# Performance work log

Hardware: AMD Instinct MI355X
Metric: run time of the kernel (lower is better)

The kernel has to match this reference:

```python
import jax, jax.numpy as jnp
import numpy as np

# Config mirroring sample_tokens(temperature=1.0, top_p=0.9, top_k=50, neg_entropy=True)
TEMPERATURE = 1.0
TOP_P = 0.9
TOP_K = 50
EPS = 1e-10


def _top_p_filter(logits, top_p):
    # Descending sort over vocab, cumulative softmax mass, shift-by-one keep rule.
    order = jnp.argsort(-logits, axis=-1)                      # [N, V]
    sorted_logits = jnp.take_along_axis(logits, order, axis=-1)
    cum = jnp.cumsum(jax.nn.softmax(sorted_logits, axis=-1), axis=-1)
    remove = cum > top_p
    # torch: sorted_indices_to_remove[...,1:] = [...,:-1]; [...,0] = 0
    remove = jnp.concatenate([jnp.zeros_like(remove[..., :1]), remove[..., :-1]], axis=-1)
    rows = jnp.arange(logits.shape[0])[:, None]
    mask = jnp.zeros(logits.shape, dtype=bool).at[rows, order].set(remove)
    return jnp.where(mask, jnp.finfo(logits.dtype).min, logits)


def _top_k_filter(logits, k):
    kth = jax.lax.top_k(logits, k)[0][..., -1:]                # k-th largest per row
    return jnp.where(logits < kth, jnp.finfo(logits.dtype).min, logits)


def setup_inputs() -> dict:
    key = jax.random.key(0)
    logits = jax.random.normal(key, (1024, 128000), dtype=jnp.float32) * 2.0
    return {"logits": logits}


def reference(logits):
    # temperature > 0 path
    z = logits / TEMPERATURE
    z = _top_p_filter(z, TOP_P)
    z = _top_k_filter(z, TOP_K)
    probs = jax.nn.softmax(z, axis=-1)                         # [N, V]
    # Categorical sample (softmax-invariant: categorical on filtered logits)
    x0 = jax.random.categorical(jax.random.key(42), z, axis=-1)  # [N] int
    initial_confidence = jnp.take_along_axis(probs, x0[:, None], axis=-1)[:, 0]
    # neg_entropy confidence: sum p * log(p + eps) over vocab
    confidence = jnp.sum(probs * jnp.log(probs + EPS), axis=-1)
    return confidence, x0, initial_confidence
```

## Files before the change

kernel.cpp:

```cpp
#include <hip/hip_runtime.h>
#include <stdint.h>


#define ROWS   1024
#define VOCAB  128000
#define CAP    2048
#define KTOP   50
#define TOPP   0.9f
#define NTHR   256
#define T0     6.0f

typedef float fx4 __attribute__((ext_vector_type(4)));

__device__ __forceinline__ void tf_round(uint32_t& x0, uint32_t& x1, int r) {
  x0 += x1;
  x1 = (x1 << r) | (x1 >> (32 - r));
  x1 ^= x0;
}

__device__ __forceinline__ uint32_t threefry_bits(uint32_t lin) {
  const uint32_t ks0 = 0u;
  const uint32_t ks1 = 42u;
  const uint32_t ks2 = 0x1BD11BDAu ^ 0u ^ 42u;
  uint32_t x0 = 0u + ks0, x1 = lin + ks1;
  tf_round(x0,x1,13); tf_round(x0,x1,15); tf_round(x0,x1,26); tf_round(x0,x1,6);
  x0 += ks1; x1 += ks2 + 1u;
  tf_round(x0,x1,17); tf_round(x0,x1,29); tf_round(x0,x1,16); tf_round(x0,x1,24);
  x0 += ks2; x1 += ks0 + 2u;
  tf_round(x0,x1,13); tf_round(x0,x1,15); tf_round(x0,x1,26); tf_round(x0,x1,6);
  x0 += ks0; x1 += ks1 + 3u;
  tf_round(x0,x1,17); tf_round(x0,x1,29); tf_round(x0,x1,16); tf_round(x0,x1,24);
  x0 += ks1; x1 += ks2 + 4u;
  tf_round(x0,x1,13); tf_round(x0,x1,15); tf_round(x0,x1,26); tf_round(x0,x1,6);
  x0 += ks2; x1 += ks0 + 5u;
  return x0 ^ x1;
}

__device__ __forceinline__ float gumbel_at(uint32_t lin) {
  uint32_t bits = threefry_bits(lin);
  float f = __uint_as_float((bits >> 9) | 0x3F800000u) - 1.0f;
  float u = f + 1.17549435e-38f;
  return -logf(-logf(u));
}

__global__ __launch_bounds__(NTHR, 4) void sampler_kernel(
    const float* __restrict__ logits, float* __restrict__ out) {
  const int row = blockIdx.x;
  const int tid = threadIdx.x;
  const float* __restrict__ rowp = logits + (size_t)row * VOCAB;

  __shared__ float cand_val[CAP];
  __shared__ int   cand_idx[CAP];
  __shared__ float red_a[NTHR];
  __shared__ float red_b[NTHR];
  __shared__ int   red_i[NTHR];
  __shared__ int   s_cnt;
  __shared__ float s_topv[KTOP];
  __shared__ int   s_tops[KTOP];

  if (tid == 0) s_cnt = 0;
  __syncthreads();

  float m0 = -__builtin_inff(), m1 = -__builtin_inff();
  float s0 = 0.f, s1 = 0.f, s2 = 0.f, s3 = 0.f;

  const fx4* __restrict__ rowp4 = reinterpret_cast<const fx4*>(rowp);

#define PROCESS(v, f4idx)                                                     \
  do {                                                                        \
    s0 += __expf((v).x); s1 += __expf((v).y);                                 \
    s2 += __expf((v).z); s3 += __expf((v).w);                                 \
    m0 = fmaxf(m0, fmaxf((v).x, (v).y));                                      \
    m1 = fmaxf(m1, fmaxf((v).z, (v).w));                                      \
    int hit = (((v).x >= T0) ? 1 : 0) | (((v).y >= T0) ? 2 : 0)               \
            | (((v).z >= T0) ? 4 : 0) | (((v).w >= T0) ? 8 : 0);              \
    if (hit) {                                                                \
      float xs[4] = {(v).x, (v).y, (v).z, (v).w};                             \
      _Pragma("unroll")                                                       \
      for (int j = 0; j < 4; ++j) {                                           \
        if (hit & (1 << j)) {                                                 \
          int slot = atomicAdd(&s_cnt, 1);                                    \
          if (slot < CAP) { cand_val[slot] = xs[j]; cand_idx[slot] = 4*(f4idx) + j; } \
        }                                                                     \
      }                                                                       \
    }                                                                         \
  } while (0)

#define LOADG(dst, base)                                                      \
  do {                                                                        \
    dst##0 = __builtin_nontemporal_load(&rowp4[(base)]);                      \
    dst##1 = __builtin_nontemporal_load(&rowp4[(base) + 256]);                \
    dst##2 = __builtin_nontemporal_load(&rowp4[(base) + 512]);                \
    dst##3 = __builtin_nontemporal_load(&rowp4[(base) + 768]);                \
  } while (0)

#define PROCG(src, base)                                                      \
  do {                                                                        \
    PROCESS(src##0, (base));                                                  \
    PROCESS(src##1, (base) + 256);                                            \
    PROCESS(src##2, (base) + 512);                                            \
    PROCESS(src##3, (base) + 768);                                            \
  } while (0)

  fx4 A0, A1, A2, A3, B0, B1, B2, B3;
  LOADG(A, tid);
  LOADG(B, 1024 + tid);

  for (int t = 0; t < 14; ++t) {
    const int gA = 2 * t;
    PROCG(A, gA * 1024 + tid);
    LOADG(A, (gA + 2) * 1024 + tid);
    __builtin_amdgcn_sched_barrier(0);
    PROCG(B, (gA + 1) * 1024 + tid);
    LOADG(B, (gA + 3) * 1024 + tid);
    __builtin_amdgcn_sched_barrier(0);
  }
  fx4 TL = __builtin_nontemporal_load(&rowp4[31744 + tid]);
  PROCG(A, 28672 + tid);
  LOADG(A, 30720 + tid);
  __builtin_amdgcn_sched_barrier(0);
  PROCG(B, 29696 + tid);
  PROCG(A, 30720 + tid);
  PROCESS(TL, 31744 + tid);
#undef PROCG
#undef LOADG
#undef PROCESS

  red_a[tid] = (s0 + s1) + (s2 + s3);
  red_b[tid] = fmaxf(m0, m1);
  __syncthreads();
  for (int off = NTHR/2; off > 0; off >>= 1) {
    if (tid < off) {
      red_a[tid] += red_a[tid + off];
      red_b[tid] = fmaxf(red_b[tid], red_b[tid + off]);
    }
    __syncthreads();
  }
  const float S = red_a[0];
  const float m = red_b[0];

  int total = s_cnt;
  if (total < KTOP || total > CAP) {
    float delta = 2.0f;
    float Tt = m - delta;
    for (int attempt = 0; attempt < 20; ++attempt) {
      Tt = m - delta;
      int c_loc = 0;
      for (int i = tid; i < VOCAB; i += NTHR) c_loc += (rowp[i] >= Tt) ? 1 : 0;
      red_i[tid] = c_loc;
      __syncthreads();
      for (int off = NTHR/2; off > 0; off >>= 1) {
        if (tid < off) red_i[tid] += red_i[tid + off];
        __syncthreads();
      }
      int tot = red_i[0];
      __syncthreads();
      if (tot >= KTOP && tot <= CAP) break;
      delta = (tot < KTOP) ? delta * 2.0f : delta * 0.7f;
    }
    if (tid == 0) s_cnt = 0;
    __syncthreads();
    for (int i = tid; i < VOCAB; i += NTHR) {
      float x = rowp[i];
      if (x >= Tt) {
        int slot = atomicAdd(&s_cnt, 1);
        if (slot < CAP) { cand_val[slot] = x; cand_idx[slot] = i; }
      }
    }
    __syncthreads();
    total = s_cnt;
  }
  const int cnt = total < CAP ? total : CAP;

  if (cnt == 0) {
    if (tid == 0) { out[row] = 0.f; out[ROWS+row] = 0.f; out[2*ROWS+row] = 0.f; }
    return;
  }
  const int nsel = cnt < KTOP ? cnt : KTOP;

  for (int c = tid; c < cnt; c += NTHR) {
    float v = cand_val[c]; int ci = cand_idx[c];
    int r = 0;
    for (int d = 0; d < cnt; ++d) {
      float vd = cand_val[d];
      int   id = cand_idx[d];
      r += ((vd > v) || (vd == v && id < ci)) ? 1 : 0;
    }
    if (r < KTOP) { s_topv[r] = v; s_tops[r] = ci; }
  }
  __syncthreads();

  if (tid < 64) {
    const int lane = tid;
    const bool act = lane < nsel;
    float v  = act ? s_topv[lane] : -__builtin_inff();
    int  col = act ? s_tops[lane] : 0x7FFFFFFF;
    float e  = act ? __expf(v) : 0.0f;
    float p  = e / S;

    float csum = p;
#pragma unroll
    for (int off = 1; off < 64; off <<= 1) {
      float t = __shfl_up(csum, off);
      if (lane >= off) csum += t;
    }
    float prev = __shfl_up(csum, 1);
    bool keep = act && (lane == 0 || prev <= TOPP);

    float ek = keep ? e : 0.0f;
    float Sp = ek;
#pragma unroll
    for (int off = 32; off > 0; off >>= 1) Sp += __shfl_xor(Sp, off);

    float pk = keep ? e / Sp : 0.0f;
    float ct = keep ? pk * logf(pk + 1e-10f) : 0.0f;
    float conf = ct;
#pragma unroll
    for (int off = 32; off > 0; off >>= 1) conf += __shfl_xor(conf, off);

    const uint32_t rowbase = (uint32_t)row * (uint32_t)VOCAB;
    float g = keep ? (v + gumbel_at(rowbase + (uint32_t)col)) : -__builtin_inff();
    float bg = g; int bc = col; float bp = pk;
#pragma unroll
    for (int off = 32; off > 0; off >>= 1) {
      float og = __shfl_xor(bg, off);
      int   oc = __shfl_xor(bc, off);
      float op = __shfl_xor(bp, off);
      if (og > bg || (og == bg && oc < bc)) { bg = og; bc = oc; bp = op; }
    }

    if (lane == 0) {
      out[row]          = conf;
      out[ROWS + row]   = (float)bc;
      out[2*ROWS + row] = bp;
    }
  }
}

extern "C" void kernel_launch(void* const* d_in, const int* in_sizes, int n_in,
                              void* d_out, int out_size, void* d_ws, size_t ws_size,
                              hipStream_t stream) {
  const float* logits = (const float*)d_in[0];
  float* out = (float*)d_out;
  sampler_kernel<<<ROWS, NTHR, 0, stream>>>(logits, out);
}
```

Baseline: 631.6 us.

## Raise occupancy with smaller load groups, fewer accumulators, and smaller candidate buffer

Doubles the launch-bounds occupancy target from 4 to 8 blocks per CU. To make that fit, it shrinks the candidate buffer in shared memory, halves the per-thread load group from four to two float4 vectors, and merges the four exp-sum accumulators into two. Nontemporal loads are replaced by plain loads. This trades per-thread memory-level parallelism for more resident waves to hide latency on a bandwidth-bound streaming pass, and it risks more rows falling back to the slow recount path because of the smaller candidate capacity.

```diff
diff --git a/kernel.cpp b/kernel.cpp
--- a/kernel.cpp
+++ b/kernel.cpp
@@ -4,7 +4,7 @@
 
 #define ROWS   1024
 #define VOCAB  128000
-#define CAP    2048
+#define CAP    1536
 #define KTOP   50
 #define TOPP   0.9f
 #define NTHR   256
@@ -43,7 +43,7 @@
   return -logf(-logf(u));
 }
 
-__global__ __launch_bounds__(NTHR, 4) void sampler_kernel(
+__global__ __launch_bounds__(NTHR, 8) void sampler_kernel(
     const float* __restrict__ logits, float* __restrict__ out) {
   const int row = blockIdx.x;
   const int tid = threadIdx.x;
@@ -62,14 +62,14 @@
   __syncthreads();
 
   float m0 = -__builtin_inff(), m1 = -__builtin_inff();
-  float s0 = 0.f, s1 = 0.f, s2 = 0.f, s3 = 0.f;
+  float s0 = 0.f, s1 = 0.f;
 
   const fx4* __restrict__ rowp4 = reinterpret_cast<const fx4*>(rowp);
 
 #define PROCESS(v, f4idx)                                                     \
   do {                                                                        \
     s0 += __expf((v).x); s1 += __expf((v).y);                                 \
-    s2 += __expf((v).z); s3 += __expf((v).w);                                 \
+    s0 += __expf((v).z); s1 += __expf((v).w);                                 \
     m0 = fmaxf(m0, fmaxf((v).x, (v).y));                                      \
     m1 = fmaxf(m1, fmaxf((v).z, (v).w));                                      \
     int hit = (((v).x >= T0) ? 1 : 0) | (((v).y >= T0) ? 2 : 0)               \
@@ -86,47 +86,40 @@
     }                                                                         \
   } while (0)
 
-#define LOADG(dst, base)                                                      \
+#define LOADG2(dst, base)                                                     \
   do {                                                                        \
-    dst##0 = __builtin_nontemporal_load(&rowp4[(base)]);                      \
-    dst##1 = __builtin_nontemporal_load(&rowp4[(base) + 256]);                \
-    dst##2 = __builtin_nontemporal_load(&rowp4[(base) + 512]);                \
-    dst##3 = __builtin_nontemporal_load(&rowp4[(base) + 768]);                \
+    dst##0 = rowp4[(base)];                                                   \
+    dst##1 = rowp4[(base) + 256];                                             \
   } while (0)
 
-#define PROCG(src, base)                                                      \
+#define PROCG2(src, base)                                                     \
   do {                                                                        \
     PROCESS(src##0, (base));                                                  \
     PROCESS(src##1, (base) + 256);                                            \
-    PROCESS(src##2, (base) + 512);                                            \
-    PROCESS(src##3, (base) + 768);                                            \
   } while (0)
 
-  fx4 A0, A1, A2, A3, B0, B1, B2, B3;
-  LOADG(A, tid);
-  LOADG(B, 1024 + tid);
-
-  for (int t = 0; t < 14; ++t) {
+  fx4 A0, A1, B0, B1;
+  LOADG2(A, tid);
+  LOADG2(B, 512 + tid);
+
+  for (int t = 0; t < 30; ++t) {
     const int gA = 2 * t;
-    PROCG(A, gA * 1024 + tid);
-    LOADG(A, (gA + 2) * 1024 + tid);
+    PROCG2(A, gA * 512 + tid);
+    LOADG2(A, (gA + 2) * 512 + tid);
     __builtin_amdgcn_sched_barrier(0);
-    PROCG(B, (gA + 1) * 1024 + tid);
-    LOADG(B, (gA + 3) * 1024 + tid);
+    PROCG2(B, (gA + 1) * 512 + tid);
+    LOADG2(B, (gA + 3) * 512 + tid);
     __builtin_amdgcn_sched_barrier(0);
   }
-  fx4 TL = __builtin_nontemporal_load(&rowp4[31744 + tid]);
-  PROCG(A, 28672 + tid);
-  LOADG(A, 30720 + tid);
-  __builtin_amdgcn_sched_barrier(0);
-  PROCG(B, 29696 + tid);
-  PROCG(A, 30720 + tid);
+  fx4 TL = rowp4[31744 + tid];
+  PROCG2(A, 30720 + tid);
+  PROCG2(B, 31232 + tid);
   PROCESS(TL, 31744 + tid);
-#undef PROCG
-#undef LOADG
+#undef PROCG2
+#undef LOADG2
 #undef PROCESS
 
-  red_a[tid] = (s0 + s1) + (s2 + s3);
+  red_a[tid] = s0 + s1;
   red_b[tid] = fmaxf(m0, m1);
   __syncthreads();
   for (int off = NTHR/2; off > 0; off >>= 1) {
```

Result: slower. 672.4 us (+6.5%).
